# Optimization experiments

Hardware: AMD Instinct MI355X
Metric: run time of the kernel (lower is better)

Reference implementation:

```python
import jax, jax.numpy as jnp
import numpy as np

N, FIN, FOUT = 4096, 512, 256
ALPHA = 0.2          # LeakyReLU negative slope
NEG_INF = -9e15      # mask value from the torch source


def setup_inputs() -> dict:
    key = jax.random.key(0)
    ks = jax.random.split(key, 11)
    h = jax.random.normal(ks[0], (N, FIN), dtype=jnp.float32)
    adj_n = jax.random.randint(ks[1], (N, N), 0, 2, dtype=jnp.int32)
    adj_d = jax.random.randint(ks[2], (N, N), 0, 2, dtype=jnp.int32)
    G_nd = jax.random.normal(ks[3], (2, N, FOUT), dtype=jnp.float32)
    # learned parameters (xavier-ish scale)
    W_n = jax.random.normal(ks[4], (FIN, FOUT), dtype=jnp.float32) * 0.05
    a1_n = jax.random.normal(ks[5], (FOUT, 1), dtype=jnp.float32) * 0.05
    a2_n = jax.random.normal(ks[6], (FOUT, 1), dtype=jnp.float32) * 0.05
    W_d = jax.random.normal(ks[7], (FIN, FOUT), dtype=jnp.float32) * 0.05
    a1_d = jax.random.normal(ks[8], (FOUT, 1), dtype=jnp.float32) * 0.05
    a2_d = jax.random.normal(ks[9], (FOUT, 1), dtype=jnp.float32) * 0.05
    scale = jnp.zeros((1,), dtype=jnp.float32)
    return {"h": h, "adj_n": adj_n, "adj_d": adj_d, "G_nd": G_nd,
            "W_n": W_n, "a1_n": a1_n, "a2_n": a2_n,
            "W_d": W_d, "a1_d": a1_d, "a2_d": a2_d, "scale": scale}


def _gat(h, adj, W, a1, a2):
    # Wh: [N, FOUT]
    Wh = h @ W
    # outer-sum attention logits: e[i,j] = leakyrelu(Wh_i.a1 + Wh_j.a2)
    e = jax.nn.leaky_relu((Wh @ a1) + (Wh @ a2).T, negative_slope=ALPHA)  # [N, N]
    att = jnp.where(adj > 0, e, jnp.float32(NEG_INF))
    att = jax.nn.softmax(att, axis=-1)
    # dropout is identity in eval mode
    return jax.nn.elu(att @ Wh)  # [N, FOUT]


def reference(h, adj_n, adj_d, G_nd, W_n, a1_n, a2_n, W_d, a1_d, a2_d, scale):
    f_n_S = _gat(h, adj_n, W_n, a1_n, a2_n)
    f_d_S = _gat(h, adj_d, W_d, a1_d, a2_d)
    # The G_nd cross-attention branch (f_nd_C) in the torch source is computed
    # but never used in the returned value; omitted here (jit would DCE it).
    return f_n_S + f_d_S
```

## Files before the change

### kernel.cpp

```cpp
#include <hip/hip_runtime.h>

#define N_NODES 4096
#define FIN     512
#define FOUT    256
#define NSPLIT  4
#define NTILES  ((N_NODES / NSPLIT) / 64)

typedef __attribute__((ext_vector_type(8))) short bf16x8s;
typedef __attribute__((ext_vector_type(4))) float f32x4;
typedef __attribute__((ext_vector_type(8))) unsigned short u16x8;
typedef unsigned short u16;
typedef unsigned int   u32;

__device__ inline u16 f2b(float f) {
    union { float f; unsigned int u; } v; v.f = f;
    unsigned int r = v.u + 0x7fffu + ((v.u >> 16) & 1u);
    return (u16)(r >> 16);
}

__global__ __launch_bounds__(256) void prep_kernel(
    const float* __restrict__ h, const float* __restrict__ Wn,
    const float* __restrict__ Wd,
    u16* __restrict__ hb, u16* __restrict__ WTb, float* __restrict__ s12)
{
    __shared__ u16 tl[64 * 72];
    const int t = threadIdx.x;
    const int bid = blockIdx.x;

    if (bid < 1024) {
        int idx = (bid * 256 + t) * 8;
        float4 f0 = *(const float4*)&h[idx];
        float4 f1 = *(const float4*)&h[idx + 4];
        u16x8 o;
        o[0]=f2b(f0.x); o[1]=f2b(f0.y); o[2]=f2b(f0.z); o[3]=f2b(f0.w);
        o[4]=f2b(f1.x); o[5]=f2b(f1.y); o[6]=f2b(f1.z); o[7]=f2b(f1.w);
        *(u16x8*)&hb[idx] = o;
    } else if (bid < 1088) {
        int id = bid - 1024;
        int kx = id & 7, ny = (id >> 3) & 3, b = id >> 5;
        const float* W = b ? Wd : Wn;
        int k0 = kx * 64, n0 = ny * 64;
        int kr = t >> 2, nc0 = (t & 3) * 16;
        const float* src = W + (size_t)(k0 + kr) * FOUT + n0 + nc0;
        #pragma unroll
        for (int jv = 0; jv < 4; ++jv) {
            float4 f = *(const float4*)(src + jv * 4);
            tl[(nc0 + jv * 4 + 0) * 72 + kr] = f2b(f.x);
            tl[(nc0 + jv * 4 + 1) * 72 + kr] = f2b(f.y);
            tl[(nc0 + jv * 4 + 2) * 72 + kr] = f2b(f.z);
            tl[(nc0 + jv * 4 + 3) * 72 + kr] = f2b(f.w);
        }
        __syncthreads();
        int n = t >> 2, kc0 = (t & 3) * 16;
        u16* dst = WTb + ((size_t)b << 17) + (size_t)(n0 + n) * FIN + k0 + kc0;
        *(uint4*)dst       = *(uint4*)&tl[n * 72 + kc0];
        *(uint4*)(dst + 8) = *(uint4*)&tl[n * 72 + kc0 + 8];
    } else {
        float4 z = {0.f, 0.f, 0.f, 0.f};
        float4* p4 = (float4*)s12;
        #pragma unroll
        for (int k = 0; k < 16; ++k) p4[k * 256 + t] = z;
    }
}

__global__ __launch_bounds__(256) void wh_gemm_kernel(
    const u16* __restrict__ hb, const u16* __restrict__ WTb,
    const float* __restrict__ a1n, const float* __restrict__ a2n,
    const float* __restrict__ a1d, const float* __restrict__ a2d,
    u16* __restrict__ WhT, float* __restrict__ s1, float* __restrict__ s2)
{
    __shared__ u16 smem[8192];
    u16* a_lds = smem;
    u16* b_lds = smem + 4096;

    const int t = threadIdx.x, lane = t & 63, w = t >> 6;
    const int q = lane >> 4, ln = lane & 15;
    const int i0 = blockIdx.x * 64, n0 = blockIdx.y * 64, b = blockIdx.z;
    const u16* wt = WTb + ((size_t)b << 17);

    f32x4 acc[4];
    #pragma unroll
    for (int i = 0; i < 4; ++i) acc[i] = (f32x4){0.f, 0.f, 0.f, 0.f};

    for (int kt = 0; kt < 8; ++kt) {
        const int k0 = kt * 64;
        __syncthreads();
        #pragma unroll
        for (int it = 0; it < 2; ++it) {
            int chunk = it * 256 + t;
            int r = chunk >> 3, kc = chunk & 7;
            const u16* g = hb + (size_t)(i0 + r) * FIN + k0 + ((kc ^ (r & 7)) * 8);
            u16* l = a_lds + (it * 256 + w * 64) * 8;
            __builtin_amdgcn_global_load_lds(
                (const __attribute__((address_space(1))) void*)g,
                (__attribute__((address_space(3))) void*)l, 16, 0, 0);
        }
        #pragma unroll
        for (int it = 0; it < 2; ++it) {
            int chunk = it * 256 + t;
            int n = chunk >> 3, kc = chunk & 7;
            const u16* g = wt + (size_t)(n0 + n) * FIN + k0 + ((kc ^ (n & 7)) * 8);
            u16* l = b_lds + (it * 256 + w * 64) * 8;
            __builtin_amdgcn_global_load_lds(
                (const __attribute__((address_space(1))) void*)g,
                (__attribute__((address_space(3))) void*)l, 16, 0, 0);
        }
        __syncthreads();
        #pragma unroll
        for (int ks = 0; ks < 2; ++ks) {
            int sw = ((ks * 4 + q) ^ (ln & 7)) * 8;
            bf16x8s af = *(const bf16x8s*)&a_lds[(w * 16 + ln) * 64 + sw];
            #pragma unroll
            for (int nt = 0; nt < 4; ++nt) {
                bf16x8s bfv = *(const bf16x8s*)&b_lds[(nt * 16 + ln) * 64 + sw];
                acc[nt] = __builtin_amdgcn_mfma_f32_16x16x32_bf16(af, bfv, acc[nt], 0, 0, 0);
            }
        }
    }

    {
        const float* a1 = b ? a1d : a1n;
        const float* a2 = b ? a2d : a2n;
        float s1p[4] = {0.f, 0.f, 0.f, 0.f};
        float s2p[4] = {0.f, 0.f, 0.f, 0.f};
        #pragma unroll
        for (int nt = 0; nt < 4; ++nt) {
            float va1 = a1[n0 + nt * 16 + ln];
            float va2 = a2[n0 + nt * 16 + ln];
            #pragma unroll
            for (int r = 0; r < 4; ++r) {
                s1p[r] += acc[nt][r] * va1;
                s2p[r] += acc[nt][r] * va2;
            }
        }
        #pragma unroll
        for (int r = 0; r < 4; ++r) {
            #pragma unroll
            for (int off = 8; off >= 1; off >>= 1) {
                s1p[r] += __shfl_xor(s1p[r], off);
                s2p[r] += __shfl_xor(s2p[r], off);
            }
            if (ln == 0) {
                int row = i0 + w * 16 + q * 4 + r;
                atomicAdd(&s1[b * N_NODES + row], s1p[r]);
                atomicAdd(&s2[b * N_NODES + row], s2p[r]);
            }
        }
    }

    __syncthreads();
    #pragma unroll
    for (int nt = 0; nt < 4; ++nt)
        #pragma unroll
        for (int r = 0; r < 4; ++r)
            smem[(nt * 16 + ln) * 72 + (w * 16 + q * 4 + r)] = f2b(acc[nt][r]);
    __syncthreads();
    {
        const int nl = t >> 2, is = (t & 3) * 16;
        u16* dst = WhT + ((size_t)b << 20) + (size_t)(n0 + nl) * N_NODES + i0 + is;
        *(uint4*)dst       = *(uint4*)&smem[nl * 72 + is];
        *(uint4*)(dst + 8) = *(uint4*)&smem[nl * 72 + is + 8];
    }
}

__global__ __launch_bounds__(256) void attn_kernel(
    const int* __restrict__ adj_n, const int* __restrict__ adj_d,
    const u16* __restrict__ WhT,
    const float* __restrict__ s1, const float* __restrict__ s2,
    float* __restrict__ num_ws, float* __restrict__ den_ws)
{
    __shared__ u16 wht_lds[256 * 64];
    __shared__ u16 p_lds[64 * 64];
    __shared__ float den_lds[64];

    const int t = threadIdx.x, lane = t & 63, w = t >> 6;
    const int q = lane >> 4, ln = lane & 15;
    const int b = blockIdx.z, split = blockIdx.y;
    const int i0 = blockIdx.x * 64;

    const int* adjb = b ? adj_d : adj_n;
    const u16* whtB = WhT + ((size_t)b << 20);
    const float* s1b = s1 + b * N_NODES;
    const float* s2b = s2 + b * N_NODES;

    const int pr = t >> 3;
    const int cw = t & 7;
    const int pc = cw * 8;
    const float s1v0 = s1b[i0 + pr];
    const float s1v1 = s1b[i0 + pr + 32];
    const size_t arow0 = (size_t)(i0 + pr) * N_NODES + pc;
    const size_t arow1 = arow0 + (size_t)32 * N_NODES;

    if (t < 64) den_lds[t] = 0.f;

    f32x4 acc[4][4];
    #pragma unroll
    for (int mt = 0; mt < 4; ++mt)
        #pragma unroll
        for (int nt = 0; nt < 4; ++nt) acc[mt][nt] = (f32x4){0.f, 0.f, 0.f, 0.f};

    const int jbase = split * (N_NODES / NSPLIT);
    int4 a00_pf = *(const int4*)&adjb[arow0 + jbase];
    int4 a01_pf = *(const int4*)&adjb[arow0 + jbase + 4];
    int4 a10_pf = *(const int4*)&adjb[arow1 + jbase];
    int4 a11_pf = *(const int4*)&adjb[arow1 + jbase + 4];
    float4 sv0_pf = *(const float4*)&s2b[jbase + pc];
    float4 sv1_pf = *(const float4*)&s2b[jbase + pc + 4];

    for (int jt = 0; jt < NTILES; ++jt) {
        const int j0 = jbase + jt * 64;
        __syncthreads();
        #pragma unroll
        for (int it = 0; it < 8; ++it) {
            int chunk = it * 256 + t;
            int n = chunk >> 3, kc = chunk & 7;
            const u16* g = whtB + (size_t)n * N_NODES + j0 + ((kc ^ (n & 7)) * 8);
            u16* l = wht_lds + (it * 256 + w * 64) * 8;
            __builtin_amdgcn_global_load_lds(
                (const __attribute__((address_space(1))) void*)g,
                (__attribute__((address_space(3))) void*)l, 16, 0, 0);
        }
        int4 a00 = a00_pf, a01 = a01_pf, a10 = a10_pf, a11 = a11_pf;
        float4 sv0 = sv0_pf, sv1 = sv1_pf;
        if (jt < NTILES - 1) {
            const int jn = j0 + 64;
            a00_pf = *(const int4*)&adjb[arow0 + jn];
            a01_pf = *(const int4*)&adjb[arow0 + jn + 4];
            a10_pf = *(const int4*)&adjb[arow1 + jn];
            a11_pf = *(const int4*)&adjb[arow1 + jn + 4];
            sv0_pf = *(const float4*)&s2b[jn + pc];
            sv1_pf = *(const float4*)&s2b[jn + pc + 4];
        }
        int v0[8] = {a00.x, a00.y, a00.z, a00.w, a01.x, a01.y, a01.z, a01.w};
        int v1[8] = {a10.x, a10.y, a10.z, a10.w, a11.x, a11.y, a11.z, a11.w};
        float svf[8] = {sv0.x, sv0.y, sv0.z, sv0.w, sv1.x, sv1.y, sv1.z, sv1.w};
        float d0 = 0.f, d1 = 0.f;
        u16x8 pk0, pk1;
        #pragma unroll
        for (int jj = 0; jj < 8; ++jj) {
            float sv = svf[jj];
            float x0 = s1v0 + sv, x1 = s1v1 + sv;
            float p0 = (v0[jj] > 0) ? __expf(fmaxf(x0, 0.2f * x0)) : 0.f;
            float p1 = (v1[jj] > 0) ? __expf(fmaxf(x1, 0.2f * x1)) : 0.f;
            d0 += p0; d1 += p1;
            pk0[jj] = f2b(p0); pk1[jj] = f2b(p1);
        }
        d0 += __shfl_down(d0, 4, 8); d1 += __shfl_down(d1, 4, 8);
        d0 += __shfl_down(d0, 2, 8); d1 += __shfl_down(d1, 2, 8);
        d0 += __shfl_down(d0, 1, 8); d1 += __shfl_down(d1, 1, 8);
        if ((t & 7) == 0) { den_lds[pr] += d0; den_lds[pr + 32] += d1; }
        int swp = ((cw ^ (pr & 7)) * 8);
        *(u16x8*)&p_lds[pr * 64 + swp] = pk0;
        *(u16x8*)&p_lds[(pr + 32) * 64 + swp] = pk1;
        __syncthreads();
        #pragma unroll
        for (int ks = 0; ks < 2; ++ks) {
            int sw = ((ks * 4 + q) ^ (ln & 7)) * 8;
            bf16x8s af[4];
            #pragma unroll
            for (int mt = 0; mt < 4; ++mt)
                af[mt] = *(const bf16x8s*)&p_lds[(mt * 16 + ln) * 64 + sw];
            #pragma unroll
            for (int nt = 0; nt < 4; ++nt) {
                bf16x8s bfv = *(const bf16x8s*)&wht_lds[(w * 64 + nt * 16 + ln) * 64 + sw];
                #pragma unroll
                for (int mt = 0; mt < 4; ++mt)
                    acc[mt][nt] = __builtin_amdgcn_mfma_f32_16x16x32_bf16(af[mt], bfv, acc[mt][nt], 0, 0, 0);
            }
        }
    }
    const size_t pbase = (size_t)(b * NSPLIT + split) * N_NODES;
    #pragma unroll
    for (int mt = 0; mt < 4; ++mt)
        #pragma unroll
        for (int r = 0; r < 4; ++r) {
            int row = mt * 16 + q * 4 + r;
            #pragma unroll
            for (int nt = 0; nt < 4; ++nt)
                num_ws[(pbase + i0 + row) * FOUT + w * 64 + nt * 16 + ln] = acc[mt][nt][r];
        }
    if (t < 64) den_ws[pbase + i0 + t] = den_lds[t];
}

__global__ __launch_bounds__(256) void reduce_kernel(
    const float* __restrict__ num_ws, const float* __restrict__ den_ws,
    float* __restrict__ out)
{
    int gid = blockIdx.x * 256 + threadIdx.x;
    int i = gid >> 6;
    int f4 = (gid & 63) * 4;
    float4 o = {0.f, 0.f, 0.f, 0.f};
    #pragma unroll
    for (int b = 0; b < 2; ++b) {
        float4 num = {0.f, 0.f, 0.f, 0.f};
        float den = 0.f;
        #pragma unroll
        for (int s = 0; s < NSPLIT; ++s) {
            const float4 v = *(const float4*)&num_ws[((size_t)(b * NSPLIT + s) * N_NODES + i) * FOUT + f4];
            num.x += v.x; num.y += v.y; num.z += v.z; num.w += v.w;
            den += den_ws[(size_t)(b * NSPLIT + s) * N_NODES + i];
        }
        float inv = 1.0f / den;
        float e0 = num.x * inv, e1 = num.y * inv, e2 = num.z * inv, e3 = num.w * inv;
        o.x += (e0 > 0.f) ? e0 : expm1f(e0);
        o.y += (e1 > 0.f) ? e1 : expm1f(e1);
        o.z += (e2 > 0.f) ? e2 : expm1f(e2);
        o.w += (e3 > 0.f) ? e3 : expm1f(e3);
    }
    *(float4*)&out[(size_t)i * FOUT + f4] = o;
}

extern "C" void kernel_launch(void* const* d_in, const int* in_sizes, int n_in,
                              void* d_out, int out_size, void* d_ws, size_t ws_size,
                              hipStream_t stream) {
    const float* h    = (const float*)d_in[0];
    const int*   adjn = (const int*)d_in[1];
    const int*   adjd = (const int*)d_in[2];
    const float* Wn   = (const float*)d_in[4];
    const float* a1n  = (const float*)d_in[5];
    const float* a2n  = (const float*)d_in[6];
    const float* Wd   = (const float*)d_in[7];
    const float* a1d  = (const float*)d_in[8];
    const float* a2d  = (const float*)d_in[9];

    char* ws = (char*)d_ws;
    u16*  WhT  = (u16*)ws;
    float* s1  = (float*)(ws + ((size_t)8 << 20));
    float* s2  = s1 + 2 * N_NODES;
    float* den = s2 + 2 * N_NODES;
    u16*  hb   = (u16*)(ws + ((size_t)8 << 20) + ((size_t)256 << 10));
    u16*  WTb  = (u16*)(ws + ((size_t)12 << 20) + ((size_t)256 << 10));
    float* num = (float*)(ws + ((size_t)8 << 20) + ((size_t)256 << 10));

    prep_kernel<<<1089, 256, 0, stream>>>(h, Wn, Wd, hb, WTb, s1);
    wh_gemm_kernel<<<dim3(64, 4, 2), 256, 0, stream>>>(hb, WTb, a1n, a2n, a1d, a2d, WhT, s1, s2);
    attn_kernel<<<dim3(64, NSPLIT, 2), 256, 0, stream>>>(adjn, adjd, WhT, s1, s2, num, den);
    reduce_kernel<<<1024, 256, 0, stream>>>(num, den, (float*)d_out);
}
```

Measured before the change: 204.0 us.

## Raise attention split count to 8 and keep denominators in registers

The attention kernel now takes a runtime split count and uses 8 splits along the neighbour dimension when the workspace is large enough, otherwise 4. This doubles the grid to 1024 blocks to improve occupancy on the GPU's many compute units. The per-tile shuffle reduction and shared-memory accumulation of softmax denominators are replaced by per-thread register accumulators that are reduced once at the end. The next-tile adjacency prefetch is moved after the barrier. The cost is twice as many partial numerators for the reduce kernel to read and a larger workspace footprint.

```diff
diff --git a/kernel.cpp b/kernel.cpp
--- a/kernel.cpp
+++ b/kernel.cpp
@@ -3,8 +3,6 @@
 #define N_NODES 4096
 #define FIN     512
 #define FOUT    256
-#define NSPLIT  4
-#define NTILES  ((N_NODES / NSPLIT) / 64)
 
 typedef __attribute__((ext_vector_type(8))) short bf16x8s;
 typedef __attribute__((ext_vector_type(4))) float f32x4;
@@ -167,16 +165,18 @@
     const int* __restrict__ adj_n, const int* __restrict__ adj_d,
     const u16* __restrict__ WhT,
     const float* __restrict__ s1, const float* __restrict__ s2,
-    float* __restrict__ num_ws, float* __restrict__ den_ws)
+    float* __restrict__ num_ws, float* __restrict__ den_ws, int nsplit)
 {
-    __shared__ u16 wht_lds[256 * 64];
-    __shared__ u16 p_lds[64 * 64];
-    __shared__ float den_lds[64];
+    __shared__ u16 smem_all[20480];
+    u16* wht_lds = smem_all;
+    u16* p_lds   = smem_all + 16384;
 
     const int t = threadIdx.x, lane = t & 63, w = t >> 6;
     const int q = lane >> 4, ln = lane & 15;
     const int b = blockIdx.z, split = blockIdx.y;
     const int i0 = blockIdx.x * 64;
+    const int jcount = N_NODES / nsplit;
+    const int ntiles = jcount / 64;
 
     const int* adjb = b ? adj_d : adj_n;
     const u16* whtB = WhT + ((size_t)b << 20);
@@ -191,7 +191,7 @@
     const size_t arow0 = (size_t)(i0 + pr) * N_NODES + pc;
     const size_t arow1 = arow0 + (size_t)32 * N_NODES;
 
-    if (t < 64) den_lds[t] = 0.f;
+    float den0 = 0.f, den1 = 0.f;
 
     f32x4 acc[4][4];
     #pragma unroll
@@ -199,7 +199,7 @@
         #pragma unroll
         for (int nt = 0; nt < 4; ++nt) acc[mt][nt] = (f32x4){0.f, 0.f, 0.f, 0.f};
 
-    const int jbase = split * (N_NODES / NSPLIT);
+    const int jbase = split * jcount;
     int4 a00_pf = *(const int4*)&adjb[arow0 + jbase];
     int4 a01_pf = *(const int4*)&adjb[arow0 + jbase + 4];
     int4 a10_pf = *(const int4*)&adjb[arow1 + jbase];
@@ -207,7 +207,7 @@
     float4 sv0_pf = *(const float4*)&s2b[jbase + pc];
     float4 sv1_pf = *(const float4*)&s2b[jbase + pc + 4];
 
-    for (int jt = 0; jt < NTILES; ++jt) {
+    for (int jt = 0; jt < ntiles; ++jt) {
         const int j0 = jbase + jt * 64;
         __syncthreads();
         #pragma unroll
@@ -220,9 +220,24 @@
                 (const __attribute__((address_space(1))) void*)g,
                 (__attribute__((address_space(3))) void*)l, 16, 0, 0);
         }
-        int4 a00 = a00_pf, a01 = a01_pf, a10 = a10_pf, a11 = a11_pf;
-        float4 sv0 = sv0_pf, sv1 = sv1_pf;
-        if (jt < NTILES - 1) {
+        int v0[8] = {a00_pf.x, a00_pf.y, a00_pf.z, a00_pf.w, a01_pf.x, a01_pf.y, a01_pf.z, a01_pf.w};
+        int v1[8] = {a10_pf.x, a10_pf.y, a10_pf.z, a10_pf.w, a11_pf.x, a11_pf.y, a11_pf.z, a11_pf.w};
+        float svf[8] = {sv0_pf.x, sv0_pf.y, sv0_pf.z, sv0_pf.w, sv1_pf.x, sv1_pf.y, sv1_pf.z, sv1_pf.w};
+        u16x8 pk0, pk1;
+        #pragma unroll
+        for (int jj = 0; jj < 8; ++jj) {
+            float sv = svf[jj];
+            float x0 = s1v0 + sv, x1 = s1v1 + sv;
+            float p0 = (v0[jj] > 0) ? __expf(fmaxf(x0, 0.2f * x0)) : 0.f;
+            float p1 = (v1[jj] > 0) ? __expf(fmaxf(x1, 0.2f * x1)) : 0.f;
+            den0 += p0; den1 += p1;
+            pk0[jj] = f2b(p0); pk1[jj] = f2b(p1);
+        }
+        int swp = ((cw ^ (pr & 7)) * 8);
+        *(u16x8*)&p_lds[pr * 64 + swp] = pk0;
+        *(u16x8*)&p_lds[(pr + 32) * 64 + swp] = pk1;
+        __syncthreads();
+        if (jt + 1 < ntiles) {
             const int jn = j0 + 64;
             a00_pf = *(const int4*)&adjb[arow0 + jn];
             a01_pf = *(const int4*)&adjb[arow0 + jn + 4];
@@ -231,28 +246,6 @@
             sv0_pf = *(const float4*)&s2b[jn + pc];
             sv1_pf = *(const float4*)&s2b[jn + pc + 4];
         }
-        int v0[8] = {a00.x, a00.y, a00.z, a00.w, a01.x, a01.y, a01.z, a01.w};
-        int v1[8] = {a10.x, a10.y, a10.z, a10.w, a11.x, a11.y, a11.z, a11.w};
-        float svf[8] = {sv0.x, sv0.y, sv0.z, sv0.w, sv1.x, sv1.y, sv1.z, sv1.w};
-        float d0 = 0.f, d1 = 0.f;
-        u16x8 pk0, pk1;
-        #pragma unroll
-        for (int jj = 0; jj < 8; ++jj) {
-            float sv = svf[jj];
-            float x0 = s1v0 + sv, x1 = s1v1 + sv;
-            float p0 = (v0[jj] > 0) ? __expf(fmaxf(x0, 0.2f * x0)) : 0.f;
-            float p1 = (v1[jj] > 0) ? __expf(fmaxf(x1, 0.2f * x1)) : 0.f;
-            d0 += p0; d1 += p1;
-            pk0[jj] = f2b(p0); pk1[jj] = f2b(p1);
-        }
-        d0 += __shfl_down(d0, 4, 8); d1 += __shfl_down(d1, 4, 8);
-        d0 += __shfl_down(d0, 2, 8); d1 += __shfl_down(d1, 2, 8);
-        d0 += __shfl_down(d0, 1, 8); d1 += __shfl_down(d1, 1, 8);
-        if ((t & 7) == 0) { den_lds[pr] += d0; den_lds[pr + 32] += d1; }
-        int swp = ((cw ^ (pr & 7)) * 8);
-        *(u16x8*)&p_lds[pr * 64 + swp] = pk0;
-        *(u16x8*)&p_lds[(pr + 32) * 64 + swp] = pk1;
-        __syncthreads();
         #pragma unroll
         for (int ks = 0; ks < 2; ++ks) {
             int sw = ((ks * 4 + q) ^ (ln & 7)) * 8;
@@ -269,7 +262,14 @@
             }
         }
     }
-    const size_t pbase = (size_t)(b * NSPLIT + split) * N_NODES;
+    den0 += __shfl_down(den0, 4, 8); den1 += __shfl_down(den1, 4, 8);
+    den0 += __shfl_down(den0, 2, 8); den1 += __shfl_down(den1, 2, 8);
+    den0 += __shfl_down(den0, 1, 8); den1 += __shfl_down(den1, 1, 8);
+    const size_t pbase = (size_t)(b * nsplit + split) * N_NODES;
+    if ((t & 7) == 0) {
+        den_ws[pbase + i0 + pr] = den0;
+        den_ws[pbase + i0 + pr + 32] = den1;
+    }
     #pragma unroll
     for (int mt = 0; mt < 4; ++mt)
         #pragma unroll
@@ -279,12 +279,11 @@
             for (int nt = 0; nt < 4; ++nt)
                 num_ws[(pbase + i0 + row) * FOUT + w * 64 + nt * 16 + ln] = acc[mt][nt][r];
         }
-    if (t < 64) den_ws[pbase + i0 + t] = den_lds[t];
 }
 
 __global__ __launch_bounds__(256) void reduce_kernel(
     const float* __restrict__ num_ws, const float* __restrict__ den_ws,
-    float* __restrict__ out)
+    float* __restrict__ out, int nsplit)
 {
     int gid = blockIdx.x * 256 + threadIdx.x;
     int i = gid >> 6;
@@ -294,11 +293,10 @@
     for (int b = 0; b < 2; ++b) {
         float4 num = {0.f, 0.f, 0.f, 0.f};
         float den = 0.f;
-        #pragma unroll
-        for (int s = 0; s < NSPLIT; ++s) {
-            const float4 v = *(const float4*)&num_ws[((size_t)(b * NSPLIT + s) * N_NODES + i) * FOUT + f4];
+        for (int s = 0; s < nsplit; ++s) {
+            const float4 v = *(const float4*)&num_ws[((size_t)(b * nsplit + s) * N_NODES + i) * FOUT + f4];
             num.x += v.x; num.y += v.y; num.z += v.z; num.w += v.w;
-            den += den_ws[(size_t)(b * NSPLIT + s) * N_NODES + i];
+            den += den_ws[(size_t)(b * nsplit + s) * N_NODES + i];
         }
         float inv = 1.0f / den;
         float e0 = num.x * inv, e1 = num.y * inv, e2 = num.z * inv, e3 = num.w * inv;
@@ -328,12 +326,16 @@
     float* s1  = (float*)(ws + ((size_t)8 << 20));
     float* s2  = s1 + 2 * N_NODES;
     float* den = s2 + 2 * N_NODES;
-    u16*  hb   = (u16*)(ws + ((size_t)8 << 20) + ((size_t)256 << 10));
-    u16*  WTb  = (u16*)(ws + ((size_t)12 << 20) + ((size_t)256 << 10));
-    float* num = (float*)(ws + ((size_t)8 << 20) + ((size_t)256 << 10));
+    size_t num_off = ((size_t)8 << 20) + ((size_t)400 << 10);
+    u16*  hb   = (u16*)(ws + num_off);
+    u16*  WTb  = (u16*)(ws + num_off + ((size_t)4 << 20));
+    float* num = (float*)(ws + num_off);
+
+    const size_t per_split = (size_t)2 * N_NODES * FOUT * sizeof(float);
+    int nsplit = (ws_size >= num_off + 8 * per_split) ? 8 : 4;
 
     prep_kernel<<<1089, 256, 0, stream>>>(h, Wn, Wd, hb, WTb, s1);
     wh_gemm_kernel<<<dim3(64, 4, 2), 256, 0, stream>>>(hb, WTb, a1n, a2n, a1d, a2d, WhT, s1, s2);
-    attn_kernel<<<dim3(64, NSPLIT, 2), 256, 0, stream>>>(adjn, adjd, WhT, s1, s2, num, den);
-    reduce_kernel<<<1024, 256, 0, stream>>>(num, den, (float*)d_out);
-}
+    attn_kernel<<<dim3(64, nsplit, 2), 256, 0, stream>>>(adjn, adjd, WhT, s1, s2, num, den, nsplit);
+    reduce_kernel<<<1024, 256, 0, stream>>>(num, den, (float*)d_out, nsplit);
+}
```

After: 215.1 us. +5.4%, slower.

## Double-buffer WhT and P tiles in LDS with one barrier per tile

Applied to the files above, without the earlier changes.

The attention kernel now double-buffers the WhT and probability tiles in LDS. It issues the next tile's global-to-LDS loads after a single barrier that uses a manual vmcnt/lgkmcnt wait, and prefetches adjacency and s2 values two tiles ahead. The softmax denominators are kept in registers and reduced once at the end instead of being accumulated in LDS every tile, and the workspace offsets are moved. The goal is to hide global load latency behind the MFMA work and cut barriers, at the cost of doubled LDS use (which may lower occupancy) and a fragile hand-written waitcnt.

```diff
diff --git a/kernel.cpp b/kernel.cpp
--- a/kernel.cpp
+++ b/kernel.cpp
@@ -10,7 +10,6 @@
 typedef __attribute__((ext_vector_type(4))) float f32x4;
 typedef __attribute__((ext_vector_type(8))) unsigned short u16x8;
 typedef unsigned short u16;
-typedef unsigned int   u32;
 
 __device__ inline u16 f2b(float f) {
     union { float f; unsigned int u; } v; v.f = f;
@@ -169,9 +168,8 @@
     const float* __restrict__ s1, const float* __restrict__ s2,
     float* __restrict__ num_ws, float* __restrict__ den_ws)
 {
-    __shared__ u16 wht_lds[256 * 64];
-    __shared__ u16 p_lds[64 * 64];
-    __shared__ float den_lds[64];
+    __shared__ u16 wht_lds[2][16384];
+    __shared__ u16 p_lds[2][4096];
 
     const int t = threadIdx.x, lane = t & 63, w = t >> 6;
     const int q = lane >> 4, ln = lane & 15;
@@ -191,7 +189,7 @@
     const size_t arow0 = (size_t)(i0 + pr) * N_NODES + pc;
     const size_t arow1 = arow0 + (size_t)32 * N_NODES;
 
-    if (t < 64) den_lds[t] = 0.f;
+    float den0 = 0.f, den1 = 0.f;
 
     f32x4 acc[4][4];
     #pragma unroll
@@ -200,76 +198,103 @@
         for (int nt = 0; nt < 4; ++nt) acc[mt][nt] = (f32x4){0.f, 0.f, 0.f, 0.f};
 
     const int jbase = split * (N_NODES / NSPLIT);
-    int4 a00_pf = *(const int4*)&adjb[arow0 + jbase];
-    int4 a01_pf = *(const int4*)&adjb[arow0 + jbase + 4];
-    int4 a10_pf = *(const int4*)&adjb[arow1 + jbase];
-    int4 a11_pf = *(const int4*)&adjb[arow1 + jbase + 4];
-    float4 sv0_pf = *(const float4*)&s2b[jbase + pc];
-    float4 sv1_pf = *(const float4*)&s2b[jbase + pc + 4];
+
+    #pragma unroll
+    for (int it = 0; it < 8; ++it) {
+        int chunk = it * 256 + t;
+        int n = chunk >> 3, kc = chunk & 7;
+        const u16* g = whtB + (size_t)n * N_NODES + jbase + ((kc ^ (n & 7)) * 8);
+        u16* l = &wht_lds[0][(it * 256 + w * 64) * 8];
+        __builtin_amdgcn_global_load_lds(
+            (const __attribute__((address_space(1))) void*)g,
+            (__attribute__((address_space(3))) void*)l, 16, 0, 0);
+    }
+    int4   apf[2][2][2];
+    float4 sv[2][2];
+    #pragma unroll
+    for (int s = 0; s < 2; ++s) {
+        const int js = jbase + s * 64;
+        apf[s][0][0] = *(const int4*)&adjb[arow0 + js];
+        apf[s][0][1] = *(const int4*)&adjb[arow0 + js + 4];
+        apf[s][1][0] = *(const int4*)&adjb[arow1 + js];
+        apf[s][1][1] = *(const int4*)&adjb[arow1 + js + 4];
+        sv[s][0] = *(const float4*)&s2b[js + pc];
+        sv[s][1] = *(const float4*)&s2b[js + pc + 4];
+    }
 
     for (int jt = 0; jt < NTILES; ++jt) {
-        const int j0 = jbase + jt * 64;
-        __syncthreads();
-        #pragma unroll
-        for (int it = 0; it < 8; ++it) {
-            int chunk = it * 256 + t;
-            int n = chunk >> 3, kc = chunk & 7;
-            const u16* g = whtB + (size_t)n * N_NODES + j0 + ((kc ^ (n & 7)) * 8);
-            u16* l = wht_lds + (it * 256 + w * 64) * 8;
-            __builtin_amdgcn_global_load_lds(
-                (const __attribute__((address_space(1))) void*)g,
-                (__attribute__((address_space(3))) void*)l, 16, 0, 0);
-        }
-        int4 a00 = a00_pf, a01 = a01_pf, a10 = a10_pf, a11 = a11_pf;
-        float4 sv0 = sv0_pf, sv1 = sv1_pf;
-        if (jt < NTILES - 1) {
-            const int jn = j0 + 64;
-            a00_pf = *(const int4*)&adjb[arow0 + jn];
-            a01_pf = *(const int4*)&adjb[arow0 + jn + 4];
-            a10_pf = *(const int4*)&adjb[arow1 + jn];
-            a11_pf = *(const int4*)&adjb[arow1 + jn + 4];
-            sv0_pf = *(const float4*)&s2b[jn + pc];
-            sv1_pf = *(const float4*)&s2b[jn + pc + 4];
-        }
-        int v0[8] = {a00.x, a00.y, a00.z, a00.w, a01.x, a01.y, a01.z, a01.w};
-        int v1[8] = {a10.x, a10.y, a10.z, a10.w, a11.x, a11.y, a11.z, a11.w};
-        float svf[8] = {sv0.x, sv0.y, sv0.z, sv0.w, sv1.x, sv1.y, sv1.z, sv1.w};
-        float d0 = 0.f, d1 = 0.f;
+        const int cur = jt & 1;
+        float svf[8] = {sv[cur][0].x, sv[cur][0].y, sv[cur][0].z, sv[cur][0].w,
+                        sv[cur][1].x, sv[cur][1].y, sv[cur][1].z, sv[cur][1].w};
+        int v0[8] = {apf[cur][0][0].x, apf[cur][0][0].y, apf[cur][0][0].z, apf[cur][0][0].w,
+                     apf[cur][0][1].x, apf[cur][0][1].y, apf[cur][0][1].z, apf[cur][0][1].w};
+        int v1[8] = {apf[cur][1][0].x, apf[cur][1][0].y, apf[cur][1][0].z, apf[cur][1][0].w,
+                     apf[cur][1][1].x, apf[cur][1][1].y, apf[cur][1][1].z, apf[cur][1][1].w};
         u16x8 pk0, pk1;
         #pragma unroll
         for (int jj = 0; jj < 8; ++jj) {
-            float sv = svf[jj];
-            float x0 = s1v0 + sv, x1 = s1v1 + sv;
+            float svx = svf[jj];
+            float x0 = s1v0 + svx, x1 = s1v1 + svx;
             float p0 = (v0[jj] > 0) ? __expf(fmaxf(x0, 0.2f * x0)) : 0.f;
             float p1 = (v1[jj] > 0) ? __expf(fmaxf(x1, 0.2f * x1)) : 0.f;
-            d0 += p0; d1 += p1;
+            den0 += p0; den1 += p1;
             pk0[jj] = f2b(p0); pk1[jj] = f2b(p1);
         }
-        d0 += __shfl_down(d0, 4, 8); d1 += __shfl_down(d1, 4, 8);
-        d0 += __shfl_down(d0, 2, 8); d1 += __shfl_down(d1, 2, 8);
-        d0 += __shfl_down(d0, 1, 8); d1 += __shfl_down(d1, 1, 8);
-        if ((t & 7) == 0) { den_lds[pr] += d0; den_lds[pr + 32] += d1; }
-        int swp = ((cw ^ (pr & 7)) * 8);
-        *(u16x8*)&p_lds[pr * 64 + swp] = pk0;
-        *(u16x8*)&p_lds[(pr + 32) * 64 + swp] = pk1;
-        __syncthreads();
+        const int swp = ((cw ^ (pr & 7)) * 8);
+        *(u16x8*)&p_lds[cur][pr * 64 + swp] = pk0;
+        *(u16x8*)&p_lds[cur][(pr + 32) * 64 + swp] = pk1;
+
+        asm volatile("s_waitcnt vmcnt(6) lgkmcnt(0)\n\ts_barrier" ::: "memory");
+
+        {
+            const int jn1 = jbase + ((jt + 1 < NTILES) ? (jt + 1) : (NTILES - 1)) * 64;
+            #pragma unroll
+            for (int it = 0; it < 8; ++it) {
+                int chunk = it * 256 + t;
+                int n = chunk >> 3, kc = chunk & 7;
+                const u16* g = whtB + (size_t)n * N_NODES + jn1 + ((kc ^ (n & 7)) * 8);
+                u16* l = &wht_lds[cur ^ 1][(it * 256 + w * 64) * 8];
+                __builtin_amdgcn_global_load_lds(
+                    (const __attribute__((address_space(1))) void*)g,
+                    (__attribute__((address_space(3))) void*)l, 16, 0, 0);
+            }
+            const int jn2 = jbase + ((jt + 2 < NTILES) ? (jt + 2) : (NTILES - 1)) * 64;
+            apf[cur][0][0] = *(const int4*)&adjb[arow0 + jn2];
+            apf[cur][0][1] = *(const int4*)&adjb[arow0 + jn2 + 4];
+            apf[cur][1][0] = *(const int4*)&adjb[arow1 + jn2];
+            apf[cur][1][1] = *(const int4*)&adjb[arow1 + jn2 + 4];
+            sv[cur][0] = *(const float4*)&s2b[jn2 + pc];
+            sv[cur][1] = *(const float4*)&s2b[jn2 + pc + 4];
+        }
+
+        const u16* wbuf = wht_lds[cur];
+        const u16* pbuf = p_lds[cur];
         #pragma unroll
         for (int ks = 0; ks < 2; ++ks) {
             int sw = ((ks * 4 + q) ^ (ln & 7)) * 8;
             bf16x8s af[4];
             #pragma unroll
             for (int mt = 0; mt < 4; ++mt)
-                af[mt] = *(const bf16x8s*)&p_lds[(mt * 16 + ln) * 64 + sw];
+                af[mt] = *(const bf16x8s*)&pbuf[(mt * 16 + ln) * 64 + sw];
             #pragma unroll
             for (int nt = 0; nt < 4; ++nt) {
-                bf16x8s bfv = *(const bf16x8s*)&wht_lds[(w * 64 + nt * 16 + ln) * 64 + sw];
+                bf16x8s bfv = *(const bf16x8s*)&wbuf[(w * 64 + nt * 16 + ln) * 64 + sw];
                 #pragma unroll
                 for (int mt = 0; mt < 4; ++mt)
-                    acc[mt][nt] = __builtin_amdgcn_mfma_f32_16x16x32_bf16(af[mt], bfv, acc[mt][nt], 0, 0, 0);
-            }
-        }
-    }
+                    acc[mt][nt] = __builtin_amdgcn_mfma_f32_16x16x32_bf16(
+                        af[mt], bfv, acc[mt][nt], 0, 0, 0);
+            }
+        }
+    }
+
+    den0 += __shfl_down(den0, 4, 8); den1 += __shfl_down(den1, 4, 8);
+    den0 += __shfl_down(den0, 2, 8); den1 += __shfl_down(den1, 2, 8);
+    den0 += __shfl_down(den0, 1, 8); den1 += __shfl_down(den1, 1, 8);
     const size_t pbase = (size_t)(b * NSPLIT + split) * N_NODES;
+    if ((t & 7) == 0) {
+        den_ws[pbase + i0 + pr] = den0;
+        den_ws[pbase + i0 + pr + 32] = den1;
+    }
     #pragma unroll
     for (int mt = 0; mt < 4; ++mt)
         #pragma unroll
@@ -279,7 +304,6 @@
             for (int nt = 0; nt < 4; ++nt)
                 num_ws[(pbase + i0 + row) * FOUT + w * 64 + nt * 16 + ln] = acc[mt][nt][r];
         }
-    if (t < 64) den_ws[pbase + i0 + t] = den_lds[t];
 }
 
 __global__ __launch_bounds__(256) void reduce_kernel(
@@ -328,9 +352,10 @@
     float* s1  = (float*)(ws + ((size_t)8 << 20));
     float* s2  = s1 + 2 * N_NODES;
     float* den = s2 + 2 * N_NODES;
-    u16*  hb   = (u16*)(ws + ((size_t)8 << 20) + ((size_t)256 << 10));
-    u16*  WTb  = (u16*)(ws + ((size_t)12 << 20) + ((size_t)256 << 10));
-    float* num = (float*)(ws + ((size_t)8 << 20) + ((size_t)256 << 10));
+    size_t num_off = ((size_t)8 << 20) + ((size_t)400 << 10);
+    u16*  hb   = (u16*)(ws + num_off);
+    u16*  WTb  = (u16*)(ws + num_off + ((size_t)4 << 20));
+    float* num = (float*)(ws + num_off);
 
     prep_kernel<<<1089, 256, 0, stream>>>(h, Wn, Wd, hb, WTb, s1);
     wh_gemm_kernel<<<dim3(64, 4, 2), 256, 0, stream>>>(hb, WTb, a1n, a2n, a1d, a2d, WhT, s1, s2);
```

Result: slower. 269.9 us (+32.3%).
